# Performance work log

Hardware: AMD Instinct MI355X
Metric: run time of the kernel (lower is better)

## Reference

```python
import jax, jax.numpy as jnp
import numpy as np

N, IN_DIM, HID, NCLS = 100000, 512, 128, 10
ALPHA = 0.2  # LeakyReLU negative slope

def _xavier_normal(key, shape, gain=1.414):
    fan_in, fan_out = shape[0], shape[1]
    std = gain * (2.0 / (fan_in + fan_out)) ** 0.5
    return (jax.random.normal(key, shape, jnp.float32) * std).astype(jnp.float32)

def setup_inputs() -> dict:
    key = jax.random.key(0)
    k1, k2, k3, k4, k5, k6 = jax.random.split(key, 6)
    features = jax.random.normal(k1, (N, IN_DIM), jnp.float32)
    # learned params per init_kwargs (xavier_normal with gain=1.414 as in torch)
    C = _xavier_normal(k2, (IN_DIM, HID))
    W = _xavier_normal(k3, (2 * HID, HID))
    V = _xavier_normal(k4, (HID, NCLS))
    # per-node top-2 neighbors from sortNodes(weight_dict[idx]); the buggy
    # `while len(...) < 2` loop never runs, so only the first merge matters.
    n1_idx = jax.random.randint(k5, (N,), 0, N, dtype=jnp.int64 if jax.config.read('jax_enable_x64') else jnp.int32)
    n2_idx = jax.random.randint(k6, (N,), 0, N, dtype=n1_idx.dtype)
    return {"features": features, "C": C, "W": W, "V": V,
            "n1_idx": n1_idx, "n2_idx": n2_idx}

def reference(features, C, W, V, n1_idx, n2_idx):
    # h = features @ C : [N, H]
    h = features @ C
    # For every node, the effective output of the Huffman merge loop is the
    # single merge of its two top-sorted neighbors (duplicated if degree 1):
    # concat(h[n1], h[n2]) @ W. Split W into halves to avoid materializing [N, 2H].
    W1, W2 = W[:HID], W[HID:]                      # each [H, H]
    outs = h[n1_idx] @ W1 + h[n2_idx] @ W2         # [N, H]
    results = jax.nn.leaky_relu(outs @ V, negative_slope=ALPHA)  # [N, num_class]
    return jax.nn.log_softmax(results, axis=1)
```

## Files before the change

### kernel.cpp

```cpp
#include <hip/hip_runtime.h>
#include <hip/hip_bf16.h>
#include <stdint.h>

#define NROWS 100000
#define INDIM 512
#define HID 128
#define NCLS 10
#define LEAKY_ALPHA 0.2f

typedef __bf16 bf16x8_t __attribute__((ext_vector_type(8)));
typedef __bf16 bf16x4_t __attribute__((ext_vector_type(4)));
typedef float f32x4_t __attribute__((ext_vector_type(4)));
typedef unsigned short ushort8_t __attribute__((ext_vector_type(8)));

union Frag {
    bf16x8_t v8;
    bf16x4_t v4[2];
    unsigned short u[8];
};

__device__ __forceinline__ unsigned short f2bf(float x) {
    union { __hip_bfloat16 b; unsigned short u; } cv;
    cv.b = __float2bfloat16(x);
    return cv.u;
}

__device__ __forceinline__ int img_addr(int r, int kk) {
    int p = r >> 1;
    int o = ((r & 1) << 6) | (kk << 1);
    return (p << 7) | ((((o >> 4) ^ (p & 7)) << 4) | (o & 15));
}

__device__ __forceinline__ void gload_lds16(const void* g, void* l) {
    __builtin_amdgcn_global_load_lds(
        (const __attribute__((address_space(1))) unsigned int*)g,
        (__attribute__((address_space(3))) unsigned int*)l, 16, 0, 0);
}

__global__ __launch_bounds__(256) void k_prep(
    const float* __restrict__ C, const float* __restrict__ W, const float* __restrict__ V,
    unsigned short* __restrict__ Qimg) {
    __shared__ float Vl[HID * NCLS];
    __shared__ float Pl[2][HID][10];
    __shared__ float Cl[64][132];

    const int tid = threadIdx.x, b = blockIdx.x;
    for (int i = tid; i < HID * NCLS; i += 256) Vl[i] = V[i];
    __syncthreads();

    {
        const int half = tid >> 7, j = tid & 127;
        const float* wr = W + (half * HID + j) * HID;
        float s[NCLS];
#pragma unroll
        for (int c = 0; c < NCLS; ++c) s[c] = 0.f;
        for (int m = 0; m < HID; m += 4) {
            float4 wv = *reinterpret_cast<const float4*>(wr + m);
            float wa[4] = {wv.x, wv.y, wv.z, wv.w};
#pragma unroll
            for (int u = 0; u < 4; ++u)
#pragma unroll
                for (int c = 0; c < NCLS; ++c) s[c] += wa[u] * Vl[(m + u) * NCLS + c];
        }
#pragma unroll
        for (int c = 0; c < NCLS; ++c) Pl[half][j][c] = s[c];
    }
    const int k0 = b << 6;
    {
        const int kr = tid >> 2, seg = (tid & 3) << 5;
        const float4* src = reinterpret_cast<const float4*>(C + (k0 + kr) * HID + seg);
#pragma unroll
        for (int j = 0; j < 8; ++j)
            *reinterpret_cast<float4*>(&Cl[kr][seg + 4 * j]) = src[j];
    }
    __syncthreads();

    for (int e = tid; e < 64 * 32; e += 256) {
        const int n = e >> 6, kl = e & 63;
        const int half = n >> 4, c = n & 15;
        float s = 0.f;
        if (c < NCLS) {
#pragma unroll 4
            for (int j = 0; j < HID; ++j) s += Cl[kl][j] * Pl[half][j][c];
        }
        const int k = k0 + kl, t = k >> 5, kk = k & 31;
        *(unsigned short*)((char*)Qimg + t * 2048 + img_addr(n, kk)) = f2bf(s);
    }
}

__global__ __launch_bounds__(256, 3) void k_gemm(
    const float* __restrict__ A,
    const unsigned short* __restrict__ Qimg,
    float* __restrict__ G)
{
    __shared__ unsigned short Qs[16384];
    __shared__ unsigned short As[2][4096];

    const int tid  = threadIdx.x;
    const int w    = tid >> 6;
    const int lane = tid & 63;
    const int l15  = lane & 15;
    const int kg   = (lane >> 4) << 2;
    const long row0 = (long)blockIdx.x * 128;

#pragma unroll
    for (int j = 0; j < 8; ++j) {
        const int off = (j * 4 + w) * 1024;
        gload_lds16((const char*)Qimg + off + lane * 16, (char*)Qs + off);
    }

    const int ar_s = tid >> 1;
    const int kh   = (tid & 1) << 4;
    long gr = row0 + ar_s;
    if (gr >= NROWS) gr = NROWS - 1;
    const float* asrc = A + gr * INDIM + kh;
    const int aw0 = img_addr(ar_s, kh);
    const int aw1 = img_addr(ar_s, kh + 8);

    int ard0[2], ard1[2], brd0[2], brd1[2];
#pragma unroll
    for (int ii = 0; ii < 2; ++ii) {
        int r = w * 32 + ii * 16 + l15;
        ard0[ii] = img_addr(r, kg);
        ard1[ii] = img_addr(r, kg + 16);
    }
#pragma unroll
    for (int f = 0; f < 2; ++f) {
        brd0[f] = img_addr(f * 16 + l15, kg);
        brd1[f] = img_addr(f * 16 + l15, kg + 16);
    }

    f32x4_t acc[2][2];
#pragma unroll
    for (int i = 0; i < 2; ++i)
#pragma unroll
        for (int f = 0; f < 2; ++f)
#pragma unroll
            for (int r = 0; r < 4; ++r) acc[i][f][r] = 0.f;

    const char* asb = (const char*)&As[0][0];
    const char* bsb = (const char*)&Qs[0];

    float4 rqA[4], rqB[4];

    {
        float4 v[4];
#pragma unroll
        for (int j = 0; j < 4; ++j) v[j] = *reinterpret_cast<const float4*>(asrc + 4 * j);
        ushort8_t lo, hi;
#pragma unroll
        for (int e = 0; e < 4; ++e) {
            lo[e] = f2bf(v[0][e]); lo[4 + e] = f2bf(v[1][e]);
            hi[e] = f2bf(v[2][e]); hi[4 + e] = f2bf(v[3][e]);
        }
        *(ushort8_t*)((char*)asb + aw0) = lo;
        *(ushort8_t*)((char*)asb + aw1) = hi;
    }
#pragma unroll
    for (int j = 0; j < 4; ++j) rqB[j] = *reinterpret_cast<const float4*>(asrc + 32 + 4 * j);
#pragma unroll
    for (int j = 0; j < 4; ++j) rqA[j] = *reinterpret_cast<const float4*>(asrc + 64 + 4 * j);
    __syncthreads();

#pragma unroll
    for (int t = 0; t < 16; ++t) {
        const int cur = t & 1;

        Frag fa[2], fb[2];
#pragma unroll
        for (int ii = 0; ii < 2; ++ii) {
            fa[ii].v4[0] = *(const bf16x4_t*)(asb + cur * 8192 + ard0[ii]);
            fa[ii].v4[1] = *(const bf16x4_t*)(asb + cur * 8192 + ard1[ii]);
        }
#pragma unroll
        for (int f = 0; f < 2; ++f) {
            fb[f].v4[0] = *(const bf16x4_t*)(bsb + t * 2048 + brd0[f]);
            fb[f].v4[1] = *(const bf16x4_t*)(bsb + t * 2048 + brd1[f]);
        }
#pragma unroll
        for (int ii = 0; ii < 2; ++ii)
#pragma unroll
            for (int f = 0; f < 2; ++f)
                acc[ii][f] = __builtin_amdgcn_mfma_f32_16x16x32_bf16(fa[ii].v8, fb[f].v8, acc[ii][f], 0, 0, 0);

        if (t < 15) {
            ushort8_t lo, hi;
            if (((t + 1) & 1) == 1) {
#pragma unroll
                for (int e = 0; e < 4; ++e) {
                    lo[e] = f2bf(rqB[0][e]); lo[4 + e] = f2bf(rqB[1][e]);
                    hi[e] = f2bf(rqB[2][e]); hi[4 + e] = f2bf(rqB[3][e]);
                }
            } else {
#pragma unroll
                for (int e = 0; e < 4; ++e) {
                    lo[e] = f2bf(rqA[0][e]); lo[4 + e] = f2bf(rqA[1][e]);
                    hi[e] = f2bf(rqA[2][e]); hi[4 + e] = f2bf(rqA[3][e]);
                }
            }
            *(ushort8_t*)((char*)asb + (cur ^ 1) * 8192 + aw0) = lo;
            *(ushort8_t*)((char*)asb + (cur ^ 1) * 8192 + aw1) = hi;

            if (t + 3 <= 15) {
                const float* src = asrc + (t + 3) * 32;
                if (((t + 3) & 1) == 1) {
#pragma unroll
                    for (int j = 0; j < 4; ++j) rqB[j] = *reinterpret_cast<const float4*>(src + 4 * j);
                } else {
#pragma unroll
                    for (int j = 0; j < 4; ++j) rqA[j] = *reinterpret_cast<const float4*>(src + 4 * j);
                }
            }
            __syncthreads();
        }
    }

    const int rq_ = (lane >> 4) << 2;
#pragma unroll
    for (int ii = 0; ii < 2; ++ii)
#pragma unroll
        for (int r = 0; r < 4; ++r) {
            long grow = row0 + w * 32 + ii * 16 + rq_ + r;
            if (l15 < NCLS && grow < NROWS) {
                G[grow * 20 + l15]        = acc[ii][0][r];
                G[grow * 20 + 10 + l15]   = acc[ii][1][r];
            }
        }
}

__global__ __launch_bounds__(256) void k_epi(
    const float* __restrict__ G,
    const int* __restrict__ n1, const int* __restrict__ n2,
    float* __restrict__ Out) {
    const long i = (long)blockIdx.x * 256 + threadIdx.x;
    if (i >= NROWS) return;
    const float2* g1 = (const float2*)(G + (long)n1[i] * 20);
    const float2* g2 = (const float2*)(G + (long)n2[i] * 20 + 10);

    float x[NCLS];
#pragma unroll
    for (int j = 0; j < 5; ++j) {
        float2 a = g1[j], b = g2[j];
        x[2 * j]     = a.x + b.x;
        x[2 * j + 1] = a.y + b.y;
    }
    float m = -1e30f;
#pragma unroll
    for (int c = 0; c < NCLS; ++c) {
        x[c] = (x[c] >= 0.f) ? x[c] : LEAKY_ALPHA * x[c];
        m = fmaxf(m, x[c]);
    }
    float sum = 0.f;
#pragma unroll
    for (int c = 0; c < NCLS; ++c) sum += __expf(x[c] - m);
    const float lse = m + __logf(sum);
    float2* o = (float2*)(Out + i * NCLS);
#pragma unroll
    for (int j = 0; j < 5; ++j) {
        float2 v = {x[2 * j] - lse, x[2 * j + 1] - lse};
        o[j] = v;
    }
}

extern "C" void kernel_launch(void* const* d_in, const int* in_sizes, int n_in,
                              void* d_out, int out_size, void* d_ws, size_t ws_size,
                              hipStream_t stream) {
    const float* features = (const float*)d_in[0];
    const float* C  = (const float*)d_in[1];
    const float* W  = (const float*)d_in[2];
    const float* V  = (const float*)d_in[3];
    const int*   n1 = (const int*)d_in[4];
    const int*   n2 = (const int*)d_in[5];
    float* out = (float*)d_out;

    char* ws = (char*)d_ws;
    unsigned short* Qimg = (unsigned short*)ws;
    float* G = (float*)(ws + 32768);

    hipLaunchKernelGGL(k_prep, dim3(8), dim3(256), 0, stream, C, W, V, Qimg);
    hipLaunchKernelGGL(k_gemm, dim3((NROWS + 127) / 128), dim3(256), 0, stream,
                       features, Qimg, G);
    hipLaunchKernelGGL(k_epi, dim3((NROWS + 255) / 256), dim3(256), 0, stream,
                       G, n1, n2, out);
}
```

Before: 64.40 us.

## Load A fragments directly from global into registers, drop LDS staging

```diff
diff --git a/kernel.cpp b/kernel.cpp
--- a/kernel.cpp
+++ b/kernel.cpp
@@ -88,13 +88,29 @@
     }
 }
 
+#define LOADC(dst, t)                                                        \
+    dst[0] = *reinterpret_cast<const float4*>(a0 + (t) * 32);                \
+    dst[1] = *reinterpret_cast<const float4*>(a0 + (t) * 32 + 16);           \
+    dst[2] = *reinterpret_cast<const float4*>(a1 + (t) * 32);                \
+    dst[3] = *reinterpret_cast<const float4*>(a1 + (t) * 32 + 16);
+
+#define CVT(fa, s)                                                           \
+    {                                                                        \
+        _Pragma("unroll")                                                    \
+        for (int e = 0; e < 4; ++e) {                                        \
+            fa[0].u[e]     = f2bf(s[0][e]);                                  \
+            fa[0].u[4 + e] = f2bf(s[1][e]);                                  \
+            fa[1].u[e]     = f2bf(s[2][e]);                                  \
+            fa[1].u[4 + e] = f2bf(s[3][e]);                                  \
+        }                                                                    \
+    }
+
 __global__ __launch_bounds__(256, 3) void k_gemm(
     const float* __restrict__ A,
     const unsigned short* __restrict__ Qimg,
     float* __restrict__ G)
 {
     __shared__ unsigned short Qs[16384];
-    __shared__ unsigned short As[2][4096];
 
     const int tid  = threadIdx.x;
     const int w    = tid >> 6;
@@ -109,21 +125,12 @@
         gload_lds16((const char*)Qimg + off + lane * 16, (char*)Qs + off);
     }
 
-    const int ar_s = tid >> 1;
-    const int kh   = (tid & 1) << 4;
-    long gr = row0 + ar_s;
-    if (gr >= NROWS) gr = NROWS - 1;
-    const float* asrc = A + gr * INDIM + kh;
-    const int aw0 = img_addr(ar_s, kh);
-    const int aw1 = img_addr(ar_s, kh + 8);
-
-    int ard0[2], ard1[2], brd0[2], brd1[2];
-#pragma unroll
-    for (int ii = 0; ii < 2; ++ii) {
-        int r = w * 32 + ii * 16 + l15;
-        ard0[ii] = img_addr(r, kg);
-        ard1[ii] = img_addr(r, kg + 16);
-    }
+    long r0 = row0 + w * 32 + l15;      if (r0 >= NROWS) r0 = NROWS - 1;
+    long r1 = r0 + 16;                  if (r1 >= NROWS) r1 = NROWS - 1;
+    const float* a0 = A + r0 * INDIM + kg;
+    const float* a1 = A + r1 * INDIM + kg;
+
+    int brd0[2], brd1[2];
 #pragma unroll
     for (int f = 0; f < 2; ++f) {
         brd0[f] = img_addr(f * 16 + l15, kg);
@@ -138,40 +145,28 @@
 #pragma unroll
             for (int r = 0; r < 4; ++r) acc[i][f][r] = 0.f;
 
-    const char* asb = (const char*)&As[0][0];
     const char* bsb = (const char*)&Qs[0];
 
-    float4 rqA[4], rqB[4];
-
-    {
-        float4 v[4];
-#pragma unroll
-        for (int j = 0; j < 4; ++j) v[j] = *reinterpret_cast<const float4*>(asrc + 4 * j);
-        ushort8_t lo, hi;
-#pragma unroll
-        for (int e = 0; e < 4; ++e) {
-            lo[e] = f2bf(v[0][e]); lo[4 + e] = f2bf(v[1][e]);
-            hi[e] = f2bf(v[2][e]); hi[4 + e] = f2bf(v[3][e]);
-        }
-        *(ushort8_t*)((char*)asb + aw0) = lo;
-        *(ushort8_t*)((char*)asb + aw1) = hi;
-    }
-#pragma unroll
-    for (int j = 0; j < 4; ++j) rqB[j] = *reinterpret_cast<const float4*>(asrc + 32 + 4 * j);
-#pragma unroll
-    for (int j = 0; j < 4; ++j) rqA[j] = *reinterpret_cast<const float4*>(asrc + 64 + 4 * j);
+    float4 qA[4], qB[4], qC[4];
+    LOADC(qA, 0)
+    LOADC(qB, 1)
+    LOADC(qC, 2)
     __syncthreads();
 
 #pragma unroll
     for (int t = 0; t < 16; ++t) {
-        const int cur = t & 1;
-
-        Frag fa[2], fb[2];
-#pragma unroll
-        for (int ii = 0; ii < 2; ++ii) {
-            fa[ii].v4[0] = *(const bf16x4_t*)(asb + cur * 8192 + ard0[ii]);
-            fa[ii].v4[1] = *(const bf16x4_t*)(asb + cur * 8192 + ard1[ii]);
-        }
+        Frag fa[2];
+        if (t % 3 == 0)      CVT(fa, qA)
+        else if (t % 3 == 1) CVT(fa, qB)
+        else                 CVT(fa, qC)
+
+        if (t + 3 <= 15) {
+            if (t % 3 == 0)      { LOADC(qA, t + 3) }
+            else if (t % 3 == 1) { LOADC(qB, t + 3) }
+            else                 { LOADC(qC, t + 3) }
+        }
+
+        Frag fb[2];
 #pragma unroll
         for (int f = 0; f < 2; ++f) {
             fb[f].v4[0] = *(const bf16x4_t*)(bsb + t * 2048 + brd0[f]);
@@ -182,37 +177,6 @@
 #pragma unroll
             for (int f = 0; f < 2; ++f)
                 acc[ii][f] = __builtin_amdgcn_mfma_f32_16x16x32_bf16(fa[ii].v8, fb[f].v8, acc[ii][f], 0, 0, 0);
-
-        if (t < 15) {
-            ushort8_t lo, hi;
-            if (((t + 1) & 1) == 1) {
-#pragma unroll
-                for (int e = 0; e < 4; ++e) {
-                    lo[e] = f2bf(rqB[0][e]); lo[4 + e] = f2bf(rqB[1][e]);
-                    hi[e] = f2bf(rqB[2][e]); hi[4 + e] = f2bf(rqB[3][e]);
-                }
-            } else {
-#pragma unroll
-                for (int e = 0; e < 4; ++e) {
-                    lo[e] = f2bf(rqA[0][e]); lo[4 + e] = f2bf(rqA[1][e]);
-                    hi[e] = f2bf(rqA[2][e]); hi[4 + e] = f2bf(rqA[3][e]);
-                }
-            }
-            *(ushort8_t*)((char*)asb + (cur ^ 1) * 8192 + aw0) = lo;
-            *(ushort8_t*)((char*)asb + (cur ^ 1) * 8192 + aw1) = hi;
-
-            if (t + 3 <= 15) {
-                const float* src = asrc + (t + 3) * 32;
-                if (((t + 3) & 1) == 1) {
-#pragma unroll
-                    for (int j = 0; j < 4; ++j) rqB[j] = *reinterpret_cast<const float4*>(src + 4 * j);
-                } else {
-#pragma unroll
-                    for (int j = 0; j < 4; ++j) rqA[j] = *reinterpret_cast<const float4*>(src + 4 * j);
-                }
-            }
-            __syncthreads();
-        }
     }
 
     const int rq_ = (lane >> 4) << 2;
@@ -222,8 +186,8 @@
         for (int r = 0; r < 4; ++r) {
             long grow = row0 + w * 32 + ii * 16 + rq_ + r;
             if (l15 < NCLS && grow < NROWS) {
-                G[grow * 20 + l15]        = acc[ii][0][r];
-                G[grow * 20 + 10 + l15]   = acc[ii][1][r];
+                G[grow * 20 + l15]      = acc[ii][0][r];
+                G[grow * 20 + 10 + l15] = acc[ii][1][r];
             }
         }
 }
```

Measured after the change: 70.07 us. 1.09x slower.
